# Optimization experiments

Measured on AMD Instinct MI355X. Metric: run time of the kernel, lower is better.

Reference implementation:

```python
import jax, jax.numpy as jnp
import numpy as np

B, T, D, H, V, K = 64, 128, 300, 256, 30000, 16
FILTERS = [3, 4, 5]
FN = [100, 100, 100]
CLS = 5


def setup_inputs() -> dict:
    key = jax.random.key(0)
    ks = jax.random.split(key, 32)
    n = lambda i, shape, s=0.05: (jax.random.normal(ks[i], shape, jnp.float32) * s)
    inp = jax.random.randint(ks[0], (B, T), 0, V)
    emb = n(1, (V + 2, D)).at[V + 1].set(0.0)  # padding_idx row = 0
    # GRU (1 layer, bidirectional), PyTorch gate order r,z,n
    Wx_f, Wh_f = n(2, (3 * H, D)), n(3, (3 * H, H))
    bx_f, bh_f = n(4, (3 * H,)), n(5, (3 * H,))
    Wx_b, Wh_b = n(6, (3 * H, D)), n(7, (3 * H, H))
    bx_b, bh_b = n(8, (3 * H,)), n(9, (3 * H,))
    fc1c_W, fc1c_b = n(10, (D, 2 * H)), n(11, (D,))
    concept_table = n(12, (V, K, D), 0.1)
    counts = jax.random.randint(ks[13], (V,), 1, K + 1)
    concept_mask = (jnp.arange(K)[None, :] < counts[:, None])  # bool [V,K]
    conv_W0, conv_b0 = n(14, (FN[0], FILTERS[0] * 2 * D)), n(15, (FN[0],))
    conv_W1, conv_b1 = n(16, (FN[1], FILTERS[1] * 2 * D)), n(17, (FN[1],))
    conv_W2, conv_b2 = n(18, (FN[2], FILTERS[2] * 2 * D)), n(19, (FN[2],))
    fc1_W, fc1_b = n(20, (100, sum(FN))), n(21, (100,))
    fc2_W, fc2_b = n(22, (CLS, 100)), n(23, (CLS,))
    return dict(inp=inp, emb=emb, Wx_f=Wx_f, Wh_f=Wh_f, bx_f=bx_f, bh_f=bh_f,
                Wx_b=Wx_b, Wh_b=Wh_b, bx_b=bx_b, bh_b=bh_b,
                fc1c_W=fc1c_W, fc1c_b=fc1c_b,
                concept_table=concept_table, concept_mask=concept_mask,
                conv_W0=conv_W0, conv_b0=conv_b0, conv_W1=conv_W1, conv_b1=conv_b1,
                conv_W2=conv_W2, conv_b2=conv_b2,
                fc1_W=fc1_W, fc1_b=fc1_b, fc2_W=fc2_W, fc2_b=fc2_b)


def _gru_dir(x, Wx, Wh, bx, bh):
    # x: [B,T,D] -> hidden states [B,T,H]; PyTorch GRU cell math.
    xg = jnp.einsum('btd,gd->btg', x, Wx) + bx  # precompute input gates [B,T,3H]

    def step(h, xg_t):
        gh = h @ Wh.T + bh
        xr, xz, xn = jnp.split(xg_t, 3, axis=-1)
        hr, hz, hn = jnp.split(gh, 3, axis=-1)
        r = jax.nn.sigmoid(xr + hr)
        z = jax.nn.sigmoid(xz + hz)
        nn_ = jnp.tanh(xn + r * hn)
        h2 = (1.0 - z) * nn_ + z * h
        return h2, h2

    h0 = jnp.zeros((x.shape[0], Wh.shape[1]), x.dtype)
    _, ys = jax.lax.scan(step, h0, jnp.swapaxes(xg, 0, 1))
    return jnp.swapaxes(ys, 0, 1)


def _forward(inp, emb, Wx_f, Wh_f, bx_f, bh_f, Wx_b, Wh_b, bx_b, bh_b,
             fc1c_W, fc1c_b, concept_table, concept_mask,
             conv_W0, conv_b0, conv_W1, conv_b1, conv_W2, conv_b2,
             fc1_W, fc1_b, fc2_W, fc2_b):
    x = emb[inp]                                   # [B,T,D]
    hf = _gru_dir(x, Wx_f, Wh_f, bx_f, bh_f)
    hb = jnp.flip(_gru_dir(jnp.flip(x, 1), Wx_b, Wh_b, bx_b, bh_b), 1)
    out = jnp.concatenate([hf, hb], axis=-1)       # [B,T,2H]
    ctx = jnp.einsum('bth,dh->btd', out, fc1c_W) + fc1c_b  # [B,T,D] context
    # batched gather-attend-reduce over per-word concept lists
    conc = concept_table[inp]                      # [B,T,K,D]
    mask = concept_mask[inp]                       # [B,T,K] bool
    scores = jnp.einsum('btkd,btd->btk', conc, ctx)
    scores = jnp.where(mask, scores, jnp.float32(-1e30))
    attn = jax.nn.softmax(scores, axis=-1)
    concept = jnp.einsum('btk,btkd->btd', attn, conc)
    concept = jax.lax.stop_gradient(concept)       # original detaches via .data.numpy()
    feat = jnp.concatenate([ctx, concept], axis=-1)  # [B,T,2D]
    pooled = []
    for fs, W, b in ((FILTERS[0], conv_W0, conv_b0),
                     (FILTERS[1], conv_W1, conv_b1),
                     (FILTERS[2], conv_W2, conv_b2)):
        L = T - fs + 1
        # Conv1d(kernel=2D*fs, stride=2D) over flattened feat == token-window matmul
        win = jnp.concatenate([feat[:, i:i + L, :] for i in range(fs)], axis=-1)  # [B,L,fs*2D]
        c = jax.nn.relu(jnp.einsum('blk,fk->blf', win, W) + b)
        pooled.append(jnp.max(c, axis=1))          # max-pool over positions -> [B,FN]
    h = jnp.concatenate(pooled, axis=1)            # [B,300]; dropout is identity in eval
    h = h @ fc1_W.T + fc1_b
    h = h @ fc2_W.T + fc2_b
    return jax.nn.softmax(h, axis=1)


def reference(inp, emb, Wx_f, Wh_f, bx_f, bh_f, Wx_b, Wh_b, bx_b, bh_b,
              fc1c_W, fc1c_b, concept_table, concept_mask,
              conv_W0, conv_b0, conv_W1, conv_b1, conv_W2, conv_b2,
              fc1_W, fc1_b, fc2_W, fc2_b):
    return _forward(inp, emb, Wx_f, Wh_f, bx_f, bh_f, Wx_b, Wh_b, bx_b, bh_b,
                    fc1c_W, fc1c_b, concept_table, concept_mask,
                    conv_W0, conv_b0, conv_W1, conv_b1, conv_W2, conv_b2,
                    fc1_W, fc1_b, fc2_W, fc2_b)
```

## Files before the change

### kernel.cpp

```cpp
#include <hip/hip_runtime.h>


typedef unsigned short u16;
typedef unsigned int u32;
typedef __attribute__((ext_vector_type(4))) u16 u16x4;
typedef __attribute__((ext_vector_type(8))) u16 u16x8;
typedef __attribute__((ext_vector_type(8))) __bf16 bf16x8;
typedef __attribute__((ext_vector_type(4))) float f32x4;

__device__ __forceinline__ float bf2f(u16 u) {
    union { u32 i; float f; } x; x.i = ((u32)u) << 16; return x.f;
}
__device__ __forceinline__ u16 f2bf(float f) {
    union { float f; u32 i; } x; x.f = f;
    u32 r = x.i + 0x7FFFu + ((x.i >> 16) & 1u);
    return (u16)(r >> 16);
}
__device__ __forceinline__ float sigm(float x) { return 1.f / (1.f + __expf(-x)); }
__device__ __forceinline__ float tanh_(float x) {
    float e = __expf(-2.f * fabsf(x));
    float t = (1.f - e) / (1.f + e);
    return x < 0.f ? -t : t;
}
__device__ __forceinline__ void gload16(const u16* g, u16* l) {
    __builtin_amdgcn_global_load_lds(
        (const __attribute__((address_space(1))) void*)g,
        (__attribute__((address_space(3))) void*)l, 16, 0, 0);
}

__global__ __launch_bounds__(256) void detect_k(
    const u32* __restrict__ cmask_raw, int* __restrict__ flags)
{
    __shared__ int cnt1;
    if (threadIdx.x == 0) cnt1 = 0;
    __syncthreads();
    int c1 = 0;
    for (int i = threadIdx.x; i < 1024; i += 256)
        if (cmask_raw[i] > 1u) c1++;
    if (c1) atomicAdd(&cnt1, c1);
    __syncthreads();
    if (threadIdx.x == 0) flags[1] = (cnt1 > 0) ? 1 : 0;
}

struct CvtDesc { const void* src; u16* dst; int n; };
struct CvtArgs { CvtDesc d[11]; };

__global__ __launch_bounds__(256) void convert_f32(CvtArgs a)
{
    CvtDesc de = a.d[blockIdx.y];
    int i4 = (blockIdx.x * 256 + threadIdx.x) * 4;
    if (i4 >= de.n) return;
    const float* s = (const float*)de.src + i4;
    if (i4 + 4 <= de.n) {
        u16x4 o; o[0] = f2bf(s[0]); o[1] = f2bf(s[1]); o[2] = f2bf(s[2]); o[3] = f2bf(s[3]);
        *(u16x4*)(de.dst + i4) = o;
    } else {
        for (int e = 0; e < 4 && i4 + e < de.n; ++e) de.dst[i4 + e] = f2bf(s[e]);
    }
}

__global__ __launch_bounds__(256) void build_mask(
    const void* __restrict__ cmask, int* __restrict__ mask16, const int* __restrict__ flags)
{
    int v = blockIdx.x * 256 + threadIdx.x;
    if (v >= 30000) return;
    int m = 0;
    if (flags[1]) {
        const unsigned char* p = (const unsigned char*)cmask + (size_t)v * 16;
#pragma unroll
        for (int k = 0; k < 16; ++k) if (p[k]) m |= (1 << k);
    } else {
        const int* p = (const int*)cmask + (size_t)v * 16;
#pragma unroll
        for (int k = 0; k < 16; ++k) if (p[k]) m |= (1 << k);
    }
    mask16[v] = m;
}

__global__ __launch_bounds__(256) void repack_conv(
    const float* __restrict__ cw0, const float* __restrict__ cw1,
    const float* __restrict__ cw2, u16* __restrict__ wcat)
{
    const int r = blockIdx.x;
    const int d0 = threadIdx.x * 4;
    if (d0 >= 640) return;
    u16x4 o = {0, 0, 0, 0};
    if (r < 1200 && d0 < 600) {
        const float* src;
        if (r < 300)      { int f = r % 100,       i = r / 100;          src = cw0 + (size_t)f * 1800 + i * 600; }
        else if (r < 700) { int rr = r - 300, f = rr % 100, i = rr / 100; src = cw1 + (size_t)f * 2400 + i * 600; }
        else              { int rr = r - 700, f = rr % 100, i = rr / 100; src = cw2 + (size_t)f * 3000 + i * 600; }
        float4 x = *(const float4*)(src + d0);
        o[0] = f2bf(x.x); o[1] = f2bf(x.y); o[2] = f2bf(x.z); o[3] = f2bf(x.w);
    }
    *(u16x4*)(wcat + (size_t)r * 640 + d0) = o;
}

__global__ __launch_bounds__(64) void pack_wx(
    const float* __restrict__ wxf, const float* __restrict__ wxb,
    u16* __restrict__ wxpad)
{
    const int n = blockIdx.x;
    const float* src = n < 768 ? wxf + (size_t)n * 300 : wxb + (size_t)(n - 768) * 300;
    for (int c = threadIdx.x; c < 80; c += 64) {
        u16x4 o = {0, 0, 0, 0};
        if (c < 75) {
            float4 x = *(const float4*)(src + c * 4);
            o[0] = f2bf(x.x); o[1] = f2bf(x.y); o[2] = f2bf(x.z); o[3] = f2bf(x.w);
        }
        *(u16x4*)(wxpad + (size_t)n * 320 + c * 4) = o;
    }
}

__global__ __launch_bounds__(256) void build_bias(
    const float* __restrict__ bxf, const float* __restrict__ bhf,
    const float* __restrict__ bxb, const float* __restrict__ bhb,
    float* __restrict__ bias2)
{
    int c = blockIdx.x * 256 + threadIdx.x;
    if (c >= 1536) return;
    int cc = c < 768 ? c : c - 768;
    const float* bx = c < 768 ? bxf : bxb;
    const float* bh = c < 768 ? bhf : bhb;
    float v = bx[cc];
    if (cc < 512) v += bh[cc];
    bias2[c] = v;
}

__global__ __launch_bounds__(64) void stage_x(
    const int* __restrict__ inp, const float* __restrict__ emb,
    u16* __restrict__ xstage)
{
    const int tok = blockIdx.x;
    const float* src = emb + (size_t)inp[tok] * 300;
    for (int c = threadIdx.x; c < 80; c += 64) {
        u16x4 o = {0, 0, 0, 0};
        if (c < 75) {
            float4 x = *(const float4*)(src + c * 4);
            o[0] = f2bf(x.x); o[1] = f2bf(x.y); o[2] = f2bf(x.z); o[3] = f2bf(x.w);
        }
        *(u16x4*)(xstage + (size_t)tok * 320 + c * 4) = o;
    }
}

template<int EPI>
__global__ __launch_bounds__(256) void gemm128(
    const u16* __restrict__ A, const u16* __restrict__ W,
    const float* __restrict__ bias, u16* __restrict__ C,
    int Kpad, int Nout, int ldc)
{
    __shared__ __align__(16) u16 sA[128 * 32];
    __shared__ __align__(16) u16 sW[128 * 32];

    const int tid = threadIdx.x;
    const int n0 = blockIdx.x * 128;
    const int m0 = blockIdx.y * 128;

    const int l  = tid & 63;
    const int w  = tid >> 6;
    const int wm = (w >> 1) << 6;
    const int wn = (w & 1) << 6;
    const int fr = l & 15;
    const int fk = (l >> 4) << 3;

    const int srow = tid >> 2;
    const int scol = (tid & 3) << 3;

    f32x4 acc[4][4];
#pragma unroll
    for (int i = 0; i < 4; ++i)
#pragma unroll
        for (int j = 0; j < 4; ++j) acc[i][j] = (f32x4){0.f, 0.f, 0.f, 0.f};

    for (int k0 = 0; k0 < Kpad; k0 += 32) {
        __syncthreads();
#pragma unroll
        for (int i = 0; i < 2; ++i) {
            gload16(A + (size_t)(m0 + i * 64 + srow) * Kpad + k0 + scol,
                    sA + i * 2048 + tid * 8);
            gload16(W + (size_t)(n0 + i * 64 + srow) * Kpad + k0 + scol,
                    sW + i * 2048 + tid * 8);
        }
        __syncthreads();

        bf16x8 a[4], b[4];
#pragma unroll
        for (int i = 0; i < 4; ++i) {
            a[i] = *(const bf16x8*)(sA + (wm + i * 16 + fr) * 32 + fk);
            b[i] = *(const bf16x8*)(sW + (wn + i * 16 + fr) * 32 + fk);
        }
#pragma unroll
        for (int i = 0; i < 4; ++i)
#pragma unroll
            for (int j = 0; j < 4; ++j)
                acc[i][j] = __builtin_amdgcn_mfma_f32_16x16x32_bf16(a[i], b[j], acc[i][j], 0, 0, 0);
    }

    const int rb = (l >> 4) << 2;
    const int cc = l & 15;
#pragma unroll
    for (int j = 0; j < 4; ++j) {
        const int col = n0 + wn + j * 16 + cc;
        if (col < Nout) {
            const float bv = (EPI == 1) ? bias[col] : 0.f;
#pragma unroll
            for (int i = 0; i < 4; ++i) {
#pragma unroll
                for (int r = 0; r < 4; ++r) {
                    const int row = m0 + wm + i * 16 + rb + r;
                    C[(size_t)row * ldc + col] = f2bf(acc[i][j][r] + bv);
                }
            }
        }
    }
}

__global__ __launch_bounds__(256) void gemm_bt(
    const u16* __restrict__ A, const u16* __restrict__ W,
    const u16* __restrict__ bias, u16* __restrict__ Cb,
    int M, int N, int K, int lda, int ldc)
{
    __shared__ __align__(16) u16 sA[64 * 40];
    __shared__ __align__(16) u16 sW[64 * 40];

    const int tid = threadIdx.x;
    const int m0 = blockIdx.y * 64;
    const int n0 = blockIdx.x * 64;

    const int l  = tid & 63;
    const int w  = tid >> 6;
    const int wm = (w >> 1) << 5;
    const int wn = (w & 1) << 5;
    const int fr = l & 15;
    const int fk = (l >> 4) << 3;

    const int sr = tid >> 2;
    const int cb = (tid & 3) << 3;

    const size_t abase = (size_t)(m0 + sr) * (size_t)lda;
    const int  wrow   = n0 + sr;
    const bool wvalid = wrow < N;
    const size_t wbase = (size_t)wrow * (size_t)K;

    f32x4 acc00 = {0,0,0,0}, acc01 = {0,0,0,0}, acc10 = {0,0,0,0}, acc11 = {0,0,0,0};

    for (int k0 = 0; k0 < K; k0 += 32) {
        __syncthreads();
        {
            const u16* p = A + abase + k0 + cb;
            *(u16x4*)(sA + sr * 40 + cb)     = *(const u16x4*)p;
            *(u16x4*)(sA + sr * 40 + cb + 4) = *(const u16x4*)(p + 4);
        }
        {
            u16x4 v0 = {0,0,0,0}, v1 = {0,0,0,0};
            if (wvalid) {
                const u16* p = W + wbase + k0 + cb;
                v0 = *(const u16x4*)p;
                v1 = *(const u16x4*)(p + 4);
            }
            *(u16x4*)(sW + sr * 40 + cb)     = v0;
            *(u16x4*)(sW + sr * 40 + cb + 4) = v1;
        }
        __syncthreads();

        bf16x8 a0 = *(const bf16x8*)(sA + (wm + fr)      * 40 + fk);
        bf16x8 a1 = *(const bf16x8*)(sA + (wm + 16 + fr) * 40 + fk);
        bf16x8 b0 = *(const bf16x8*)(sW + (wn + fr)      * 40 + fk);
        bf16x8 b1 = *(const bf16x8*)(sW + (wn + 16 + fr) * 40 + fk);

        acc00 = __builtin_amdgcn_mfma_f32_16x16x32_bf16(a0, b0, acc00, 0, 0, 0);
        acc01 = __builtin_amdgcn_mfma_f32_16x16x32_bf16(a0, b1, acc01, 0, 0, 0);
        acc10 = __builtin_amdgcn_mfma_f32_16x16x32_bf16(a1, b0, acc10, 0, 0, 0);
        acc11 = __builtin_amdgcn_mfma_f32_16x16x32_bf16(a1, b1, acc11, 0, 0, 0);
    }

    const int rb = (l >> 4) << 2;
    const int cc = l & 15;
#define EPILOG(ACC, I, J)                                                     \
    {                                                                         \
        int col = n0 + wn + (J)*16 + cc;                                      \
        if (col < N) {                                                        \
            float bv = bf2f(bias[col]);                                       \
            _Pragma("unroll")                                                 \
            for (int r = 0; r < 4; ++r) {                                     \
                int row = m0 + wm + (I)*16 + rb + r;                          \
                if (row < M)                                                  \
                    Cb[(size_t)row * ldc + col] = f2bf(ACC[r] + bv);          \
            }                                                                 \
        }                                                                     \
    }
    EPILOG(acc00, 0, 0); EPILOG(acc01, 0, 1); EPILOG(acc10, 1, 0); EPILOG(acc11, 1, 1);
#undef EPILOG
}

#define GB 8
__global__ __launch_bounds__(512, 2) void gru_scan_mfma(
    const u16* __restrict__ xg,
    const u16* __restrict__ whf, const u16* __restrict__ whb,
    const float* __restrict__ bhf, const float* __restrict__ bhb,
    u16* __restrict__ outb)
{
    const int bg  = blockIdx.x;
    const int dir = blockIdx.y;
    const u16* wh = dir ? whb : whf;
    const float* bh = dir ? bhb : bhf;

    const int tid = threadIdx.x;
    const int w = tid >> 6;
    const int l = tid & 63;

    __shared__ __align__(16) u16 h_bf[16][264];
    __shared__ __align__(16) float gh[GB][772];

    for (int i = tid; i < 16 * 264; i += 512) ((u16*)h_bf)[i] = 0;

    bf16x8 bfr[6][8];
#pragma unroll
    for (int c = 0; c < 6; ++c)
#pragma unroll
        for (int kt = 0; kt < 8; ++kt) {
            const int n = w * 96 + c * 16 + (l & 15);
            const int k = kt * 32 + (l >> 4) * 8;
            bfr[c][kt] = *(const bf16x8*)(wh + (size_t)n * 256 + k);
        }
#pragma unroll
    for (int c = 0; c < 6; ++c)
#pragma unroll
        for (int kt = 0; kt < 8; ++kt)
            asm volatile("" : "+v"(bfr[c][kt]));

    const int qrow = (l >> 4) << 2;
    const int arow = l & 15;
    const int aofs = (l >> 4) << 3;
    const int j0 = l * 4;
    const int bglob = bg * GB + w;
    const float4 bhn4 = *(const float4*)(bh + 512 + j0);
    f32x4 hreg = {0.f, 0.f, 0.f, 0.f};

    __syncthreads();

    for (int s = 0; s < 128; ++s) {
        const int t = dir ? (127 - s) : s;

        f32x4 acc[6];
#pragma unroll
        for (int c = 0; c < 6; ++c) acc[c] = (f32x4){0.f, 0.f, 0.f, 0.f};
#pragma unroll
        for (int kt = 0; kt < 8; ++kt) {
            bf16x8 a = *(const bf16x8*)(&h_bf[arow][kt * 32 + aofs]);
#pragma unroll
            for (int c = 0; c < 6; ++c)
                acc[c] = __builtin_amdgcn_mfma_f32_16x16x32_bf16(a, bfr[c][kt], acc[c], 0, 0, 0);
        }

        const size_t tb = (size_t)(bglob * 128 + t) * 1536 + dir * 768;
        u16x4 xr4 = *(const u16x4*)(xg + tb + j0);
        u16x4 xz4 = *(const u16x4*)(xg + tb + 256 + j0);
        u16x4 xn4 = *(const u16x4*)(xg + tb + 512 + j0);

        if (qrow < GB) {
#pragma unroll
            for (int c = 0; c < 6; ++c) {
                const int col = w * 96 + c * 16 + (l & 15);
#pragma unroll
                for (int r = 0; r < 4; ++r)
                    gh[qrow + r][col] = acc[c][r];
            }
        }
        __syncthreads();

        u16x4 ho;
#pragma unroll
        for (int e = 0; e < 4; ++e) {
            const int j = j0 + e;
            float r = sigm(bf2f(xr4[e]) + gh[w][j]);
            float z = sigm(bf2f(xz4[e]) + gh[w][256 + j]);
            float n = tanh_(bf2f(xn4[e]) + r * (gh[w][512 + j] + bhn4[e]));
            float h2 = (1.f - z) * n + z * hreg[e];
            hreg[e] = h2;
            ho[e] = f2bf(h2);
        }
        *(u16x4*)(&h_bf[w][j0]) = ho;
        *(u16x4*)(outb + (size_t)(bglob * 128 + t) * 512 + dir * 256 + j0) = ho;
        __syncthreads();
    }
}
#undef GB

__global__ __launch_bounds__(256) void attn_kernel(
    const int* __restrict__ inp, const float* __restrict__ ctab,
    const int* __restrict__ mask16, u16* __restrict__ feat)
{
    const int tok = blockIdx.x;
    const int tid = threadIdx.x;
    const int v = inp[tok];

    __shared__ float ctx_s[300];
    __shared__ __align__(16) u16 conc_s[16 * 300];
    __shared__ float sc_s[16];
    __shared__ float at_s[16];

    for (int d = tid; d < 300; d += 256) ctx_s[d] = bf2f(feat[(size_t)tok * 640 + d]);
    {
        const float4* src = (const float4*)(ctab + (size_t)v * 4800);
        for (int i = tid; i < 1200; i += 256) {
            float4 x = src[i];
            u16x4 o; o[0] = f2bf(x.x); o[1] = f2bf(x.y); o[2] = f2bf(x.z); o[3] = f2bf(x.w);
            *(u16x4*)(conc_s + i * 4) = o;
        }
    }
    __syncthreads();

    const int g = tid >> 4, ln = tid & 15;
    float s = 0.f;
    for (int d = ln; d < 300; d += 16) s += bf2f(conc_s[g * 300 + d]) * ctx_s[d];
    s += __shfl_xor(s, 1); s += __shfl_xor(s, 2); s += __shfl_xor(s, 4); s += __shfl_xor(s, 8);
    if (ln == 0) sc_s[g] = ((mask16[v] >> g) & 1) ? s : -1e30f;
    __syncthreads();

    if (tid == 0) {
        float m = -1e30f;
#pragma unroll
        for (int i = 0; i < 16; ++i) m = fmaxf(m, sc_s[i]);
        float p[16]; float den = 0.f;
#pragma unroll
        for (int i = 0; i < 16; ++i) {
            float pe = (sc_s[i] <= -1e29f) ? 0.f : __expf(sc_s[i] - m);
            p[i] = pe; den += pe;
        }
        float inv = den > 0.f ? 1.f / den : 0.f;
#pragma unroll
        for (int i = 0; i < 16; ++i) at_s[i] = p[i] * inv;
    }
    __syncthreads();

    for (int d = tid; d < 340; d += 256) {
        float a = 0.f;
        if (d < 300) {
#pragma unroll
            for (int g2 = 0; g2 < 16; ++g2) a += at_s[g2] * bf2f(conc_s[g2 * 300 + d]);
        }
        feat[(size_t)tok * 640 + 300 + d] = f2bf(a);
    }
}

__global__ __launch_bounds__(128) void pool_fused(
    const u16* __restrict__ P, const u16* __restrict__ cbcat,
    float* __restrict__ pool)
{
    const int b = blockIdx.x, which = blockIdx.y, f = threadIdx.x;
    if (f >= 100) return;
    const int fs  = which == 0 ? 3 : (which == 1 ? 4 : 5);
    const int off = which == 0 ? 0 : (which == 1 ? 300 : 700);
    const int L   = 128 - fs + 1;
    const float bias = bf2f(cbcat[which * 100 + f]);
    float mm = -1e30f;
    for (int l2 = 0; l2 < L; ++l2) {
        float s = bias;
#pragma unroll 5
        for (int i = 0; i < fs; ++i)
            s += bf2f(P[(size_t)(b * 128 + l2 + i) * 1200 + off + i * 100 + f]);
        mm = fmaxf(mm, s);
    }
    pool[b * 300 + which * 100 + f] = fmaxf(mm, 0.f);
}

__global__ __launch_bounds__(128) void final_k(
    const float* __restrict__ pool,
    const u16* __restrict__ fc1W, const u16* __restrict__ fc1b,
    const u16* __restrict__ fc2W, const u16* __restrict__ fc2b,
    float* __restrict__ out)
{
    const int b = blockIdx.x, tid = threadIdx.x;
    __shared__ float ps[300], h1[100], lg[5];
    for (int d = tid; d < 300; d += 128) ps[d] = pool[b * 300 + d];
    __syncthreads();
    if (tid < 100) {
        float a = bf2f(fc1b[tid]);
        for (int k = 0; k < 300; ++k) a += bf2f(fc1W[tid * 300 + k]) * ps[k];
        h1[tid] = a;
    }
    __syncthreads();
    if (tid < 5) {
        float a = bf2f(fc2b[tid]);
        for (int k = 0; k < 100; ++k) a += bf2f(fc2W[tid * 100 + k]) * h1[k];
        lg[tid] = a;
    }
    __syncthreads();
    if (tid == 0) {
        float m = fmaxf(fmaxf(fmaxf(lg[0], lg[1]), fmaxf(lg[2], lg[3])), lg[4]);
        float e0 = __expf(lg[0] - m), e1 = __expf(lg[1] - m), e2 = __expf(lg[2] - m),
              e3 = __expf(lg[3] - m), e4 = __expf(lg[4] - m);
        float inv = 1.f / (e0 + e1 + e2 + e3 + e4);
        out[b * 5 + 0] = e0 * inv;
        out[b * 5 + 1] = e1 * inv;
        out[b * 5 + 2] = e2 * inv;
        out[b * 5 + 3] = e3 * inv;
        out[b * 5 + 4] = e4 * inv;
    }
}

extern "C" void kernel_launch(void* const* d_in, const int* in_sizes, int n_in,
                              void* d_out, int out_size, void* d_ws, size_t ws_size,
                              hipStream_t stream)
{
    (void)in_sizes; (void)n_in; (void)out_size; (void)ws_size;

    const int*  inp     = (const int*)d_in[0];
    const void* embR    = d_in[1];
    const void* WxfR    = d_in[2];
    const void* WhfR    = d_in[3];
    const void* bxfR    = d_in[4];
    const void* bhfR    = d_in[5];
    const void* WxbR    = d_in[6];
    const void* WhbR    = d_in[7];
    const void* bxbR    = d_in[8];
    const void* bhbR    = d_in[9];
    const void* fc1cWR  = d_in[10];
    const void* fc1cbR  = d_in[11];
    const void* ctabR   = d_in[12];
    const void* cmaskR  = d_in[13];
    const void* cw0R    = d_in[14];
    const void* cb0R    = d_in[15];
    const void* cw1R    = d_in[16];
    const void* cb1R    = d_in[17];
    const void* cw2R    = d_in[18];
    const void* cb2R    = d_in[19];
    const void* fc1WR   = d_in[20];
    const void* fc1bR   = d_in[21];
    const void* fc2WR   = d_in[22];
    const void* fc2bR   = d_in[23];

    char* ws = (char*)d_ws;
    size_t off = 0;
    auto alloc = [&](size_t bytes) -> char* {
        char* r = ws + off;
        off = (off + bytes + 255) & ~(size_t)255;
        return r;
    };

    u16*   xgc    = (u16*)alloc(8192ull * 1536 * 2);
    u16*   outb   = (u16*)alloc(8192ull * 512 * 2);
    u16*   feat   = (u16*)alloc(8192ull * 640 * 2);
    u16*   P      = (u16*)alloc(8192ull * 1200 * 2);
    u16*   xstage = (u16*)alloc(8192ull * 320 * 2);
    float* pool   = (float*)alloc(64ull * 300 * 4);
    int*   flags  = (int*)alloc(256);
    int*   mask16 = (int*)alloc(30000ull * 4);
    u16*   wxpad  = (u16*)alloc(1536ull * 320 * 2);
    float* bias2  = (float*)alloc(1536ull * 4);
    u16*   whfc   = (u16*)alloc(196608ull * 2);
    u16*   whbc   = (u16*)alloc(196608ull * 2);
    u16*   fc1cWc = (u16*)alloc(153600ull * 2);
    u16*   fc1cbc = (u16*)alloc(300ull * 2);
    u16*   wcat   = (u16*)alloc(1280ull * 640 * 2);
    u16*   cbcat  = (u16*)alloc(300ull * 2);
    u16*   fc1Wc  = (u16*)alloc(30000ull * 2);
    u16*   fc1bc  = (u16*)alloc(100ull * 2);
    u16*   fc2Wc  = (u16*)alloc(500ull * 2);
    u16*   fc2bc  = (u16*)alloc(8ull * 2);

    detect_k<<<1, 256, 0, stream>>>((const u32*)cmaskR, flags);

    {
        CvtArgs a{};
        a.d[0]  = { WhfR,   whfc,        196608 };
        a.d[1]  = { WhbR,   whbc,        196608 };
        a.d[2]  = { fc1cWR, fc1cWc,      153600 };
        a.d[3]  = { fc1cbR, fc1cbc,      300 };
        a.d[4]  = { cb0R,   cbcat,       100 };
        a.d[5]  = { cb1R,   cbcat + 100, 100 };
        a.d[6]  = { cb2R,   cbcat + 200, 100 };
        a.d[7]  = { fc1WR,  fc1Wc,       30000 };
        a.d[8]  = { fc1bR,  fc1bc,       100 };
        a.d[9]  = { fc2WR,  fc2Wc,       500 };
        a.d[10] = { fc2bR,  fc2bc,       5 };
        convert_f32<<<dim3(192, 11), 256, 0, stream>>>(a);
    }

    build_mask<<<118, 256, 0, stream>>>(cmaskR, mask16, flags);
    repack_conv<<<1280, 256, 0, stream>>>(
        (const float*)cw0R, (const float*)cw1R, (const float*)cw2R, wcat);
    pack_wx<<<1536, 64, 0, stream>>>((const float*)WxfR, (const float*)WxbR, wxpad);
    build_bias<<<6, 256, 0, stream>>>((const float*)bxfR, (const float*)bhfR,
                                      (const float*)bxbR, (const float*)bhbR, bias2);
    stage_x<<<8192, 64, 0, stream>>>(inp, (const float*)embR, xstage);

    gemm128<1><<<dim3(12, 64), 256, 0, stream>>>(
        xstage, wxpad, bias2, xgc, 320, 1536, 1536);

    gru_scan_mfma<<<dim3(8, 2), 512, 0, stream>>>(
        xgc, whfc, whbc, (const float*)bhfR, (const float*)bhbR, outb);

    gemm_bt<<<dim3(5, 128), 256, 0, stream>>>(
        outb, fc1cWc, fc1cbc, feat, 8192, 300, 512, 512, 640);

    attn_kernel<<<dim3(8192), 256, 0, stream>>>(inp, (const float*)ctabR, mask16, feat);

    gemm128<0><<<dim3(10, 64), 256, 0, stream>>>(
        feat, wcat, nullptr, P, 640, 1200, 1200);

    pool_fused<<<dim3(64, 3), 128, 0, stream>>>(P, cbcat, pool);

    final_k<<<dim3(64), 128, 0, stream>>>(pool, fc1Wc, fc1bc, fc2Wc, fc2bc, (float*)d_out);
}
```

Baseline: 510.1 us.

## Remap GRU weight columns so gate math runs in MFMA registers, double-buffer h

Reorders which weight rows each wave holds so every lane owns matching r, z and n gate columns in its accumulators. The gate nonlinearities can then run directly on MFMA results without a shared-memory gh round trip. The hidden state is double-buffered and the next step's input gates are prefetched into LDS, which cuts the per-step barriers from two to one. The cost is more scattered 2-byte LDS and global stores, and only the lanes with qrow<8 (half of each wave) do the gate math.

```diff
diff --git a/kernel.cpp b/kernel.cpp
--- a/kernel.cpp
+++ b/kernel.cpp
@@ -309,17 +309,17 @@
     const int w = tid >> 6;
     const int l = tid & 63;
 
-    __shared__ __align__(16) u16 h_bf[16][264];
-    __shared__ __align__(16) float gh[GB][772];
-
-    for (int i = tid; i < 16 * 264; i += 512) ((u16*)h_bf)[i] = 0;
+    __shared__ __align__(16) u16 hb[2][16][264];
+    __shared__ __align__(16) u16 xgs[2][GB][768];
+
+    for (int i = tid; i < 2 * 16 * 264; i += 512) ((u16*)hb)[i] = 0;
 
     bf16x8 bfr[6][8];
 #pragma unroll
     for (int c = 0; c < 6; ++c)
 #pragma unroll
         for (int kt = 0; kt < 8; ++kt) {
-            const int n = w * 96 + c * 16 + (l & 15);
+            const int n = (c >> 1) * 256 + w * 32 + ((c & 1) << 4) + (l & 15);
             const int k = kt * 32 + (l >> 4) * 8;
             bfr[c][kt] = *(const bf16x8*)(wh + (size_t)n * 256 + k);
         }
@@ -332,13 +332,27 @@
     const int qrow = (l >> 4) << 2;
     const int arow = l & 15;
     const int aofs = (l >> 4) << 3;
-    const int j0 = l * 4;
-    const int bglob = bg * GB + w;
-    const float4 bhn4 = *(const float4*)(bh + 512 + j0);
-    f32x4 hreg = {0.f, 0.f, 0.f, 0.f};
-
-    __syncthreads();
-
+    const int jj = w * 32 + (l & 15);
+    const float bhn0 = bh[512 + jj];
+    const float bhn1 = bh[512 + jj + 16];
+    float hreg[4][2] = {{0.f,0.f},{0.f,0.f},{0.f,0.f},{0.f,0.f}};
+
+    auto stage = [&](int tt, u16* dst) {
+#pragma unroll
+        for (int v = 0; v < 3; ++v) {
+            int e = (v * 512 + tid) * 4;
+            int b_in = e / 768;
+            int col  = e - b_in * 768;
+            const u16* src = xg + (size_t)((bg * GB + b_in) * 128 + tt) * 1536
+                             + dir * 768 + col;
+            *(u16x4*)(dst + b_in * 768 + col) = *(const u16x4*)src;
+        }
+    };
+
+    stage(dir ? 127 : 0, &xgs[0][0][0]);
+    __syncthreads();
+
+    int p = 0, q = 0;
     for (int s = 0; s < 128; ++s) {
         const int t = dir ? (127 - s) : s;
 
@@ -347,42 +361,38 @@
         for (int c = 0; c < 6; ++c) acc[c] = (f32x4){0.f, 0.f, 0.f, 0.f};
 #pragma unroll
         for (int kt = 0; kt < 8; ++kt) {
-            bf16x8 a = *(const bf16x8*)(&h_bf[arow][kt * 32 + aofs]);
+            bf16x8 a = *(const bf16x8*)(&hb[p][arow][kt * 32 + aofs]);
 #pragma unroll
             for (int c = 0; c < 6; ++c)
                 acc[c] = __builtin_amdgcn_mfma_f32_16x16x32_bf16(a, bfr[c][kt], acc[c], 0, 0, 0);
         }
 
-        const size_t tb = (size_t)(bglob * 128 + t) * 1536 + dir * 768;
-        u16x4 xr4 = *(const u16x4*)(xg + tb + j0);
-        u16x4 xz4 = *(const u16x4*)(xg + tb + 256 + j0);
-        u16x4 xn4 = *(const u16x4*)(xg + tb + 512 + j0);
+        if (s + 1 < 128) stage(dir ? (126 - s) : (s + 1), &xgs[q ^ 1][0][0]);
 
         if (qrow < GB) {
 #pragma unroll
-            for (int c = 0; c < 6; ++c) {
-                const int col = w * 96 + c * 16 + (l & 15);
-#pragma unroll
-                for (int r = 0; r < 4; ++r)
-                    gh[qrow + r][col] = acc[c][r];
+            for (int r = 0; r < 4; ++r) {
+                const int batch = qrow + r;
+                const u16* xrow = &xgs[q][batch][0];
+                u16* hrow = &hb[p ^ 1][batch][0];
+                u16* orow = outb + (size_t)((bg * GB + batch) * 128 + t) * 512 + dir * 256;
+#pragma unroll
+                for (int u = 0; u < 2; ++u) {
+                    const int j = jj + u * 16;
+                    float rg = sigm(bf2f(xrow[j])       + acc[0 + u][r]);
+                    float zg = sigm(bf2f(xrow[256 + j]) + acc[2 + u][r]);
+                    float ng = tanh_(bf2f(xrow[512 + j]) +
+                                     rg * (acc[4 + u][r] + (u ? bhn1 : bhn0)));
+                    float h2 = (1.f - zg) * ng + zg * hreg[r][u];
+                    hreg[r][u] = h2;
+                    u16 hb16 = f2bf(h2);
+                    hrow[j] = hb16;
+                    orow[j] = hb16;
+                }
             }
         }
         __syncthreads();
-
-        u16x4 ho;
-#pragma unroll
-        for (int e = 0; e < 4; ++e) {
-            const int j = j0 + e;
-            float r = sigm(bf2f(xr4[e]) + gh[w][j]);
-            float z = sigm(bf2f(xz4[e]) + gh[w][256 + j]);
-            float n = tanh_(bf2f(xn4[e]) + r * (gh[w][512 + j] + bhn4[e]));
-            float h2 = (1.f - z) * n + z * hreg[e];
-            hreg[e] = h2;
-            ho[e] = f2bf(h2);
-        }
-        *(u16x4*)(&h_bf[w][j0]) = ho;
-        *(u16x4*)(outb + (size_t)(bglob * 128 + t) * 512 + dir * 256 + j0) = ho;
-        __syncthreads();
+        p ^= 1; q ^= 1;
     }
 }
 #undef GB
```

Result: slower. 729.0 us (+42.9%).
